# Performance work log

Hardware: AMD Instinct MI355X
Metric: run time of the kernel (lower is better)

## Reference

```python
import jax, jax.numpy as jnp
import numpy as np

INPUT_SIZE = 512
SLOT_SIZE = 256
MLP_HIDDEN = 512
NUM_SLOTS = 8
NUM_ITERS = 3
EPSILON = 1e-6
LN_EPS = 1e-5


def _layernorm(x, g, b):
    m = jnp.mean(x, axis=-1, keepdims=True)
    v = jnp.mean(jnp.square(x - m), axis=-1, keepdims=True)
    return (x - m) * jax.lax.rsqrt(v + LN_EPS) * g + b


def setup_inputs() -> dict:
    key = jax.random.key(0)
    ks = jax.random.split(key, 16)
    N, B, W = 32, 64, 24
    s = 0.02
    inp = {
        "sentence": jax.random.normal(ks[0], (N, B, W, INPUT_SIZE), jnp.float32),
        "sentence_sum": jax.random.normal(ks[1], (N, B, INPUT_SIZE), jnp.float32),
        "mask": jax.random.randint(ks[2], (N, B, W), 0, 2, jnp.int32),
        "Wk": jax.random.normal(ks[3], (INPUT_SIZE, SLOT_SIZE), jnp.float32) * s,
        "bk": jnp.zeros((SLOT_SIZE,), jnp.float32),
        "Wv": jax.random.normal(ks[4], (INPUT_SIZE, SLOT_SIZE), jnp.float32) * s,
        "bv": jnp.zeros((SLOT_SIZE,), jnp.float32),
        "Wq": jax.random.normal(ks[5], (SLOT_SIZE, SLOT_SIZE), jnp.float32) * s,
        "bq": jnp.zeros((SLOT_SIZE,), jnp.float32),
        "g_ln": jnp.ones((SLOT_SIZE,), jnp.float32),
        "b_ln": jnp.zeros((SLOT_SIZE,), jnp.float32),
        "W1": jax.random.normal(ks[6], (SLOT_SIZE, MLP_HIDDEN), jnp.float32) * s,
        "b1": jnp.zeros((MLP_HIDDEN,), jnp.float32),
        "W2": jax.random.normal(ks[7], (MLP_HIDDEN, SLOT_SIZE), jnp.float32) * s,
        "b2": jnp.zeros((SLOT_SIZE,), jnp.float32),
        "Wbind": jax.random.normal(ks[8], (INPUT_SIZE, NUM_SLOTS * SLOT_SIZE), jnp.float32) * s,
        "bbind": jnp.zeros((NUM_SLOTS * SLOT_SIZE,), jnp.float32),
        "Wproj": jax.random.normal(ks[9], (2 * SLOT_SIZE, SLOT_SIZE), jnp.float32) * s,
        "bproj": jnp.zeros((SLOT_SIZE,), jnp.float32),
    }
    return inp


def reference(sentence, sentence_sum, mask, Wk, bk, Wv, bv, Wq, bq, g_ln, b_ln,
              W1, b1, W2, b2, Wbind, bbind, Wproj, bproj):
    N, B = sentence.shape[0], sentence.shape[1]
    # initial slots from the sentence summary: [N, B, NUM_SLOTS, SLOT]
    initial_slots = (sentence_sum @ Wbind + bbind).reshape(N, B, NUM_SLOTS, SLOT_SIZE)
    # additive mask on the word axis: [N, B, W, 1]
    maskf = -1e6 * (1.0 - mask.astype(jnp.float32))[..., None]
    # elu(+1) feature maps for keys; plain linear values
    k = jax.nn.elu(sentence @ Wk + bk) + 1.0  # [N,B,W,SLOT]
    v = sentence @ Wv + bv                    # [N,B,W,SLOT]

    scale = 1.0 / SLOT_SIZE
    slots = initial_slots
    for _ in range(NUM_ITERS):
        q = (slots @ Wq + bq) + initial_slots
        q = jax.nn.elu(q * (SLOT_SIZE ** -0.5)) + 1.0  # [N,B,S,SLOT]
        attn_logits = jnp.einsum('nbis,nbjs->nbij', k, q) + maskf  # [N,B,W,S]
        attn = jax.nn.softmax(attn_logits, axis=3) + EPSILON
        attn = attn / jnp.sum(attn, axis=2, keepdims=True)  # renorm over words
        updates = jnp.einsum('nbij,nbik->nbjk', attn, v)    # [N,B,S,SLOT]
        h = _layernorm(updates, g_ln, b_ln)
        h = jax.nn.relu(h @ W1 + b1) @ W2 + b2
        slots = slots + h * scale

    # dropout is identity in eval mode
    slots = jnp.concatenate([initial_slots, slots], axis=-1)
    slots = slots @ Wproj + bproj
    return slots
```

## Files before the change

### kernel.cpp

```cpp
#include <hip/hip_runtime.h>
#include <hip/hip_bf16.h>
#include <math.h>

typedef unsigned int uint;
typedef unsigned short ushort;
typedef __attribute__((ext_vector_type(8))) short bf16x8;
typedef __attribute__((ext_vector_type(4))) float f32x4;

__device__ __forceinline__ float bu2f(ushort u){ union{uint u; float f;} v; v.u = ((uint)u)<<16; return v.f; }
__device__ __forceinline__ ushort f2bu(float x){ union{float f; uint u;} v; v.f = x; uint r = (v.u + 0x7FFFu + ((v.u>>16)&1u))>>16; return (ushort)r; }
__device__ __forceinline__ uint pack2(float a, float b){ return (uint)f2bu(a) | ((uint)f2bu(b) << 16); }
__device__ __forceinline__ uint cvtpk2(float a, float b){
    uint r; asm("v_cvt_pk_bf16_f32 %0, %1, %2" : "=v"(r) : "v"(a), "v"(b)); return r;
}

#define GEPI_IS0  0
#define GEPI_Q    2
#define GEPI_RELU 3
#define GEPI_MLP2 4
#define GEPI_OUT  5

#define SWZ(r, c) (((r) << 5) + ((((c) ^ ((r) >> 1)) & 3) << 3))

template<int EPI>
__global__ __launch_bounds__(256) void gemm64(
    const ushort* __restrict__ Abf, int lda,
    const ushort* __restrict__ Bt,
    const float* __restrict__ xb0,
    float* __restrict__ fp0,
    ushort* __restrict__ up0, ushort* __restrict__ up1,
    int M, int N, int K)
{
    __shared__ ushort As[64 * 32];
    __shared__ ushort Bs[64 * 32];
    int tid = threadIdx.x;
    int wave = tid >> 6, lane = tid & 63;
    int wr = wave >> 1, wc = wave & 1;
    int quad = lane >> 4, l15 = lane & 15;
    int row0 = blockIdx.y * 64, col0 = blockIdx.x * 64;
    int sr = tid >> 2, c4 = tid & 3, sc = c4 * 8;
    int sst = SWZ(sr, c4);

    f32x4 acc[2][2];
    #pragma unroll
    for (int i = 0; i < 2; i++)
        #pragma unroll
        for (int j = 0; j < 2; j++) acc[i][j] = (f32x4){0.f, 0.f, 0.f, 0.f};

    const ushort* Ap = Abf + (size_t)(row0 + sr) * lda + sc;
    const ushort* Bp = Bt  + (size_t)(col0 + sr) * K   + sc;
    uint4 ra = *(const uint4*)Ap;
    uint4 rb = *(const uint4*)Bp;

    for (int k0 = 0; k0 < K; k0 += 32) {
        *(uint4*)&As[sst] = ra;
        *(uint4*)&Bs[sst] = rb;
        __syncthreads();
        if (k0 + 32 < K) {
            ra = *(const uint4*)(Ap + k0 + 32);
            rb = *(const uint4*)(Bp + k0 + 32);
        }
        bf16x8 af[2], bfr[2];
        #pragma unroll
        for (int mt = 0; mt < 2; mt++) {
            int ar = wr * 32 + mt * 16 + l15;
            af[mt] = *(const bf16x8*)&As[SWZ(ar, quad)];
        }
        #pragma unroll
        for (int nt = 0; nt < 2; nt++) {
            int br = wc * 32 + nt * 16 + l15;
            bfr[nt] = *(const bf16x8*)&Bs[SWZ(br, quad)];
        }
        #pragma unroll
        for (int mt = 0; mt < 2; mt++)
            #pragma unroll
            for (int nt = 0; nt < 2; nt++)
                acc[mt][nt] = __builtin_amdgcn_mfma_f32_16x16x32_bf16(
                    af[mt], bfr[nt], acc[mt][nt], 0, 0, 0);
        __syncthreads();
    }

    #pragma unroll
    for (int mt = 0; mt < 2; mt++) {
        #pragma unroll
        for (int nt = 0; nt < 2; nt++) {
            #pragma unroll
            for (int reg = 0; reg < 4; reg++) {
                int gr = row0 + wr * 32 + mt * 16 + quad * 4 + reg;
                int gc = col0 + wc * 32 + nt * 16 + l15;
                float x = acc[mt][nt][reg] + xb0[gc];
                if (EPI == GEPI_IS0) {
                    size_t srow = (size_t)gr * 8 + (gc >> 8);
                    int dim = gc & 255;
                    fp0[srow * 256 + dim] = x;
                    ushort xb = f2bu(x);
                    up0[srow * 512 + dim]       = xb;
                    up0[srow * 512 + 256 + dim] = xb;
                } else if (EPI == GEPI_Q) {
                    float y = (x + bu2f(up1[(size_t)gr * 512 + gc])) * 0.0625f;
                    y = y > 0.f ? y + 1.f : expf(y);
                    up0[(size_t)gr * 256 + gc] = f2bu(y);
                } else if (EPI == GEPI_RELU) {
                    up0[(size_t)gr * 512 + gc] = f2bu(fmaxf(x, 0.f));
                } else if (EPI == GEPI_MLP2) {
                    size_t i = (size_t)gr * 256 + gc;
                    float s = fp0[i] + x * (1.f / 256.f);
                    fp0[i] = s;
                    up0[(size_t)gr * 512 + 256 + gc] = f2bu(s);
                } else {
                    fp0[(size_t)gr * 256 + gc] = x;
                }
            }
        }
    }
}

__global__ __launch_bounds__(256) void gemm_kv64(
    const ushort* __restrict__ A0,
    const ushort* __restrict__ A1,
    const ushort* __restrict__ Bt,
    const float* __restrict__ bk, const float* __restrict__ bv,
    ushort* __restrict__ kbuf, ushort* __restrict__ vbuf, int K)
{
    __shared__ ushort As[64 * 32];
    __shared__ ushort Bs[64 * 32];
    int tid = threadIdx.x;
    int wave = tid >> 6, lane = tid & 63;
    int wr = wave >> 1, wc = wave & 1;
    int quad = lane >> 4, l15 = lane & 15;

    int bid = blockIdx.x;
    int x8  = bid & 7;
    int tt  = bid >> 3;
    int cb  = tt & 7;
    int rb  = (tt >> 3) * 8 + x8;
    int row0 = rb * 64, col0 = cb * 64;
    int sr = tid >> 2, c4 = tid & 3, sc = c4 * 8;
    int sst = SWZ(sr, c4);

    f32x4 acc[2][2];
    #pragma unroll
    for (int i = 0; i < 2; i++)
        #pragma unroll
        for (int j = 0; j < 2; j++) acc[i][j] = (f32x4){0.f, 0.f, 0.f, 0.f};

    const ushort* Ap = (row0 < 32768)
        ? (A0 + (size_t)(row0 + sr) * K + sc)
        : (A1 + (size_t)(row0 - 32768 + sr) * K + sc);
    const ushort* Bp = Bt + (size_t)(col0 + sr) * K + sc;
    uint4 ra = *(const uint4*)Ap;
    uint4 rbv = *(const uint4*)Bp;

    for (int k0 = 0; k0 < K; k0 += 32) {
        *(uint4*)&As[sst] = ra;
        *(uint4*)&Bs[sst] = rbv;
        __syncthreads();
        if (k0 + 32 < K) {
            ra  = *(const uint4*)(Ap + k0 + 32);
            rbv = *(const uint4*)(Bp + k0 + 32);
        }
        bf16x8 af[2], bfr[2];
        #pragma unroll
        for (int mt = 0; mt < 2; mt++) {
            int ar = wr * 32 + mt * 16 + l15;
            af[mt] = *(const bf16x8*)&As[SWZ(ar, quad)];
        }
        #pragma unroll
        for (int nt = 0; nt < 2; nt++) {
            int br = wc * 32 + nt * 16 + l15;
            bfr[nt] = *(const bf16x8*)&Bs[SWZ(br, quad)];
        }
        #pragma unroll
        for (int mt = 0; mt < 2; mt++)
            #pragma unroll
            for (int nt = 0; nt < 2; nt++)
                acc[mt][nt] = __builtin_amdgcn_mfma_f32_16x16x32_bf16(
                    af[mt], bfr[nt], acc[mt][nt], 0, 0, 0);
        __syncthreads();
    }

    bool isK = (col0 < 256);
    const float* __restrict__ bias = isK ? bk : bv;
    ushort* __restrict__ outp = isK ? kbuf : vbuf;
    int cbase = isK ? col0 : col0 - 256;

    #pragma unroll
    for (int mt = 0; mt < 2; mt++) {
        #pragma unroll
        for (int nt = 0; nt < 2; nt++) {
            #pragma unroll
            for (int reg = 0; reg < 4; reg++) {
                int gr = row0 + wr * 32 + mt * 16 + quad * 4 + reg;
                int gc = cbase + wc * 32 + nt * 16 + l15;
                float x = acc[mt][nt][reg] + bias[gc];
                if (isK) x = x > 0.f ? x + 1.f : expf(x);
                outp[(size_t)gr * 256 + gc] = f2bu(x);
            }
        }
    }
}

__global__ __launch_bounds__(256) void prep_kernel(
    const float* __restrict__ sentence,
    const float* __restrict__ sent_sum,
    const float* __restrict__ Wbind, const float* __restrict__ Wk,
    const float* __restrict__ Wv, const float* __restrict__ Wq,
    const float* __restrict__ W1, const float* __restrict__ W2,
    const float* __restrict__ Wproj,
    ushort* __restrict__ sentA0, ushort* __restrict__ sentA1,
    ushort* __restrict__ ssum_bf,
    ushort* __restrict__ Wbind_t, ushort* __restrict__ Wkv_t,
    ushort* __restrict__ Wq_t, ushort* __restrict__ W1_t,
    ushort* __restrict__ W2_t, ushort* __restrict__ Wproj_t)
{
    int gid = blockIdx.x * 256 + threadIdx.x;
    if (gid < 6291456) {
        float4 f = ((const float4*)sentence)[gid];
        uint2 o; o.x = cvtpk2(f.x, f.y); o.y = cvtpk2(f.z, f.w);
        if (gid < 4194304) ((uint2*)sentA0)[gid] = o;
        else               ((uint2*)sentA1)[gid - 4194304] = o;
        return;
    }
    int idx = gid - 6291456;
    if (idx < 262144) {
        float4 f = ((const float4*)sent_sum)[idx];
        uint2 o; o.x = pack2(f.x, f.y); o.y = pack2(f.z, f.w);
        ((uint2*)ssum_bf)[idx] = o; return;
    }
    idx -= 262144;
    if (idx < 1048576) { int n = idx >> 9, k = idx & 511;
        Wbind_t[idx] = f2bu(Wbind[(size_t)k * 2048 + n]); return; }
    idx -= 1048576;
    if (idx < 262144) { int n = idx >> 9, k = idx & 511;
        Wkv_t[idx] = f2bu(n < 256 ? Wk[(size_t)k * 256 + n] : Wv[(size_t)k * 256 + n - 256]); return; }
    idx -= 262144;
    if (idx < 65536) { int n = idx >> 8, k = idx & 255;
        Wq_t[idx] = f2bu(Wq[(size_t)k * 256 + n]); return; }
    idx -= 65536;
    if (idx < 131072) { int n = idx >> 8, k = idx & 255;
        W1_t[idx] = f2bu(W1[(size_t)k * 512 + n]); return; }
    idx -= 131072;
    if (idx < 131072) { int n = idx >> 9, k = idx & 511;
        W2_t[idx] = f2bu(W2[(size_t)k * 256 + n]); return; }
    idx -= 131072;
    if (idx < 131072) { int n = idx >> 9, k = idx & 511;
        Wproj_t[idx] = f2bu(Wproj[(size_t)k * 256 + n]); return; }
}

__global__ __launch_bounds__(256) void attn_kernel(
    const ushort* __restrict__ kbuf, const ushort* __restrict__ vbuf,
    const ushort* __restrict__ qbuf, const int* __restrict__ mask,
    const float* __restrict__ g_ln, const float* __restrict__ b_ln,
    ushort* __restrict__ ubuf)
{
    const int W = 24, S = 8;
    __shared__ ushort kk[24 * 264], vv[24 * 264], qsb[8 * 264];
    __shared__ float us[8 * 257];
    __shared__ float attnw[24][8];
    __shared__ float colsum[8], mean_s[8], rstd_s[8], maskf[24];

    int nb = blockIdx.x, t = threadIdx.x;
    size_t bw = (size_t)nb * W * 256, bs = (size_t)nb * S * 256;

    for (int l = t; l < 3072; l += 256) {
        int row = l >> 7, col = l & 127;
        ((uint*)kk)[row * 132 + col] = ((const uint*)(kbuf + bw))[l];
        ((uint*)vv)[row * 132 + col] = ((const uint*)(vbuf + bw))[l];
    }
    for (int l = t; l < 1024; l += 256) {
        int row = l >> 7, col = l & 127;
        ((uint*)qsb)[row * 132 + col] = ((const uint*)(qbuf + bs))[l];
    }
    if (t < W) maskf[t] = mask[(size_t)nb * W + t] ? 0.f : -1e6f;
    __syncthreads();

    if (t < W * S) {
        int i = t >> 3, j = t & 7;
        float a = 0.f;
        for (int d0 = 0; d0 < 256; d0 += 8) {
            bf16x8 kv8 = *(const bf16x8*)&kk[i * 264 + d0];
            bf16x8 qv8 = *(const bf16x8*)&qsb[j * 264 + d0];
            #pragma unroll
            for (int m = 0; m < 8; m++)
                a += bu2f((ushort)kv8[m]) * bu2f((ushort)qv8[m]);
        }
        attnw[i][j] = a + maskf[i];
    }
    __syncthreads();

    if (t < W) {
        float m = attnw[t][0];
        #pragma unroll
        for (int j = 1; j < S; j++) m = fmaxf(m, attnw[t][j]);
        float e[S]; float s = 0.f;
        #pragma unroll
        for (int j = 0; j < S; j++) { e[j] = expf(attnw[t][j] - m); s += e[j]; }
        #pragma unroll
        for (int j = 0; j < S; j++) attnw[t][j] = e[j] / s + 1e-6f;
    }
    __syncthreads();

    if (t < S) {
        float s = 0.f;
        for (int i = 0; i < W; i++) s += attnw[i][t];
        colsum[t] = s;
    }
    __syncthreads();

    {
        float acc[S] = {};
        #pragma unroll
        for (int i = 0; i < W; i++) {
            float vx = bu2f(vv[i * 264 + t]);
            float4 w0 = *(const float4*)&attnw[i][0];
            float4 w1 = *(const float4*)&attnw[i][4];
            acc[0] += w0.x * vx; acc[1] += w0.y * vx;
            acc[2] += w0.z * vx; acc[3] += w0.w * vx;
            acc[4] += w1.x * vx; acc[5] += w1.y * vx;
            acc[6] += w1.z * vx; acc[7] += w1.w * vx;
        }
        #pragma unroll
        for (int j = 0; j < S; j++) us[j * 257 + t] = acc[j] / colsum[j];
    }
    __syncthreads();

    {
        int lane = t & 63;
        #pragma unroll
        for (int jj = 0; jj < 2; jj++) {
            int j = (t >> 6) * 2 + jj;
            float x0 = us[j * 257 + lane],       x1 = us[j * 257 + lane + 64];
            float x2 = us[j * 257 + lane + 128], x3 = us[j * 257 + lane + 192];
            float p = x0 + x1 + x2 + x3;
            for (int off = 32; off; off >>= 1) p += __shfl_xor(p, off);
            float mean = p * (1.f / 256.f);
            float d0 = x0 - mean, d1 = x1 - mean, d2 = x2 - mean, d3 = x3 - mean;
            float vr = d0 * d0 + d1 * d1 + d2 * d2 + d3 * d3;
            for (int off = 32; off; off >>= 1) vr += __shfl_xor(vr, off);
            if (lane == 0) {
                mean_s[j] = mean;
                rstd_s[j] = rsqrtf(vr * (1.f / 256.f) + 1e-5f);
            }
        }
    }
    __syncthreads();

    {
        float g = g_ln[t], bb = b_ln[t];
        #pragma unroll
        for (int j = 0; j < S; j++)
            ubuf[bs + j * 256 + t] = f2bu((us[j * 257 + t] - mean_s[j]) * rstd_s[j] * g + bb);
    }
}

__global__ __launch_bounds__(256) void mega_kernel(
    const float* __restrict__ sentence, const float* __restrict__ sent_sum,
    const int*  __restrict__ mask,
    const float* __restrict__ Wk, const float* __restrict__ bk,
    const float* __restrict__ Wv, const float* __restrict__ bv,
    const float* __restrict__ Wq, const float* __restrict__ bq,
    const float* __restrict__ g_ln, const float* __restrict__ b_ln,
    const float* __restrict__ W1, const float* __restrict__ b1,
    const float* __restrict__ W2, const float* __restrict__ b2,
    const float* __restrict__ Wbind, const float* __restrict__ bbind,
    const float* __restrict__ Wproj, const float* __restrict__ bproj,
    float* __restrict__ out)
{
    const int W = 24, S = 8, D = 256, IN = 512, H = 512;
    __shared__ float seh[2048];
    __shared__ ushort kk[24 * 256];
    __shared__ ushort vv[24 * 256];
    __shared__ float is0s[8 * 256];
    __shared__ float sl[8 * 256];
    __shared__ float qv[8 * 256];
    __shared__ float attnw[24][8];
    __shared__ float colsum[8], mean_s[8], rstd_s[8], maskf[24];

    int nb = blockIdx.x, t = threadIdx.x;
    size_t sbase = (size_t)nb * W * IN;

    if (t < W) maskf[t] = mask[(size_t)nb * W + t] ? 0.f : -1e6f;
    for (int l = t; l < IN; l += 256) seh[l] = sent_sum[(size_t)nb * IN + l];
    __syncthreads();
    {
        float acc[S];
        #pragma unroll
        for (int j = 0; j < S; j++) acc[j] = bbind[j * D + t];
        for (int c = 0; c < IN; c++) {
            float sc = seh[c];
            #pragma unroll
            for (int j = 0; j < S; j++) acc[j] += sc * Wbind[(size_t)c * (S * D) + j * D + t];
        }
        #pragma unroll
        for (int j = 0; j < S; j++) { is0s[j * D + t] = acc[j]; sl[j * D + t] = acc[j]; }
    }
    {
        float ka[W], va[W];
        float bkv = bk[t], bvv = bv[t];
        #pragma unroll
        for (int i = 0; i < W; i++) { ka[i] = bkv; va[i] = bvv; }
        for (int ch = 0; ch < 8; ch++) {
            __syncthreads();
            for (int l = t; l < W * 64; l += 256) {
                int i = l >> 6, c = l & 63;
                seh[l] = sentence[sbase + (size_t)i * IN + ch * 64 + c];
            }
            __syncthreads();
            for (int c = 0; c < 64; c++) {
                int cg = ch * 64 + c;
                float wk = Wk[(size_t)cg * D + t];
                float wv = Wv[(size_t)cg * D + t];
                #pragma unroll
                for (int i = 0; i < W; i++) {
                    float s = seh[i * 64 + c];
                    ka[i] += s * wk; va[i] += s * wv;
                }
            }
        }
        #pragma unroll
        for (int i = 0; i < W; i++) {
            float kx = ka[i];
            kk[i * D + t] = f2bu(kx > 0.f ? kx + 1.f : expf(kx));
            vv[i * D + t] = f2bu(va[i]);
        }
    }
    __syncthreads();

    for (int it = 0; it < 3; it++) {
        {
            float qa[S]; float bqv = bq[t];
            #pragma unroll
            for (int j = 0; j < S; j++) qa[j] = bqv + is0s[j * D + t];
            for (int c = 0; c < D; c++) {
                float wq = Wq[(size_t)c * D + t];
                #pragma unroll
                for (int j = 0; j < S; j++) qa[j] += sl[j * D + c] * wq;
            }
            #pragma unroll
            for (int j = 0; j < S; j++) {
                float y = qa[j] * 0.0625f;
                qv[j * D + t] = y > 0.f ? y + 1.f : expf(y);
            }
        }
        __syncthreads();
        if (t < W * S) {
            int i = t >> 3, j = t & 7;
            float a = 0.f;
            #pragma unroll 8
            for (int d = 0; d < D; d++) a += bu2f(kk[i * D + d]) * qv[j * D + d];
            attnw[i][j] = a + maskf[i];
        }
        __syncthreads();
        if (t < W) {
            float m = attnw[t][0];
            #pragma unroll
            for (int j = 1; j < S; j++) m = fmaxf(m, attnw[t][j]);
            float e[S]; float s = 0.f;
            #pragma unroll
            for (int j = 0; j < S; j++) { e[j] = expf(attnw[t][j] - m); s += e[j]; }
            #pragma unroll
            for (int j = 0; j < S; j++) attnw[t][j] = e[j] / s + 1e-6f;
        }
        __syncthreads();
        if (t < S) {
            float s = 0.f;
            for (int i = 0; i < W; i++) s += attnw[i][t];
            colsum[t] = s;
        }
        __syncthreads();
        {
            float acc[S] = {};
            #pragma unroll
            for (int i = 0; i < W; i++) {
                float vx = bu2f(vv[i * D + t]);
                #pragma unroll
                for (int j = 0; j < S; j++) acc[j] += attnw[i][j] * vx;
            }
            #pragma unroll
            for (int j = 0; j < S; j++) qv[j * D + t] = acc[j] / colsum[j];
        }
        __syncthreads();
        {
            int lane = t & 63;
            #pragma unroll
            for (int jj = 0; jj < 2; jj++) {
                int j = (t >> 6) * 2 + jj;
                float x0 = qv[j * D + lane],       x1 = qv[j * D + lane + 64];
                float x2 = qv[j * D + lane + 128], x3 = qv[j * D + lane + 192];
                float p = x0 + x1 + x2 + x3;
                for (int off = 32; off; off >>= 1) p += __shfl_xor(p, off);
                float mean = p * (1.f / 256.f);
                float d0 = x0 - mean, d1 = x1 - mean, d2 = x2 - mean, d3 = x3 - mean;
                float vr = d0 * d0 + d1 * d1 + d2 * d2 + d3 * d3;
                for (int off = 32; off; off >>= 1) vr += __shfl_xor(vr, off);
                if (lane == 0) { mean_s[j] = mean; rstd_s[j] = rsqrtf(vr * (1.f / 256.f) + 1e-5f); }
            }
        }
        __syncthreads();
        {
            float g = g_ln[t], bb = b_ln[t];
            #pragma unroll
            for (int j = 0; j < S; j++)
                qv[j * D + t] = (qv[j * D + t] - mean_s[j]) * rstd_s[j] * g + bb;
        }
        __syncthreads();
        {
            float sa[S]; float b2v = b2[t];
            #pragma unroll
            for (int j = 0; j < S; j++) sa[j] = b2v;
            for (int half = 0; half < 2; half++) {
                int hcol = half * 256 + t;
                float ha[S]; float b1v = b1[hcol];
                #pragma unroll
                for (int j = 0; j < S; j++) ha[j] = b1v;
                for (int d = 0; d < D; d++) {
                    float w1 = W1[(size_t)d * H + hcol];
                    #pragma unroll
                    for (int j = 0; j < S; j++) ha[j] += qv[j * D + d] * w1;
                }
                __syncthreads();
                #pragma unroll
                for (int j = 0; j < S; j++) seh[j * D + t] = fmaxf(ha[j], 0.f);
                __syncthreads();
                for (int h = 0; h < 256; h++) {
                    float w2 = W2[(size_t)(half * 256 + h) * D + t];
                    #pragma unroll
                    for (int j = 0; j < S; j++) sa[j] += seh[j * D + h] * w2;
                }
            }
            __syncthreads();
            #pragma unroll
            for (int j = 0; j < S; j++) sl[j * D + t] += sa[j] * (1.f / 256.f);
        }
        __syncthreads();
    }
    {
        float oa[S]; float bpv = bproj[t];
        #pragma unroll
        for (int j = 0; j < S; j++) oa[j] = bpv;
        for (int c = 0; c < D; c++) {
            float wp1 = Wproj[(size_t)c * D + t];
            float wp2 = Wproj[(size_t)(D + c) * D + t];
            #pragma unroll
            for (int j = 0; j < S; j++)
                oa[j] += is0s[j * D + c] * wp1 + sl[j * D + c] * wp2;
        }
        #pragma unroll
        for (int j = 0; j < S; j++)
            out[(size_t)nb * (S * D) + j * D + t] = oa[j];
    }
}

extern "C" void kernel_launch(void* const* d_in, const int* in_sizes, int n_in,
                              void* d_out, int out_size, void* d_ws, size_t ws_size,
                              hipStream_t stream)
{
    const float* sentence = (const float*)d_in[0];
    const float* sent_sum = (const float*)d_in[1];
    const int*  mask      = (const int*)d_in[2];
    const float* Wk = (const float*)d_in[3];  const float* bk = (const float*)d_in[4];
    const float* Wv = (const float*)d_in[5];  const float* bv = (const float*)d_in[6];
    const float* Wq = (const float*)d_in[7];  const float* bq = (const float*)d_in[8];
    const float* g_ln = (const float*)d_in[9];  const float* b_ln = (const float*)d_in[10];
    const float* W1 = (const float*)d_in[11]; const float* b1 = (const float*)d_in[12];
    const float* W2 = (const float*)d_in[13]; const float* b2 = (const float*)d_in[14];
    const float* Wbind = (const float*)d_in[15]; const float* bbind = (const float*)d_in[16];
    const float* Wproj = (const float*)d_in[17]; const float* bproj = (const float*)d_in[18];
    float* out = (float*)d_out;

    const size_t WS_NEEDED = 123076608ULL;
    if (ws_size >= WS_NEEDED) {
        char* w = (char*)d_ws;
        float*  slots   = (float*) (w);
        ushort* catb    = (ushort*)(w + 16777216);
        ushort* kbuf    = (ushort*)(w + 33554432);
        ushort* vbuf    = (ushort*)(w + 58720256);
        ushort* qbuf    = (ushort*)(w + 83886080);
        ushort* ubuf    = (ushort*)(w + 92274688);
        ushort* hbuf    = (ushort*)(w + 100663296);
        ushort* ssum_bf = (ushort*)(w + 117440512);
        ushort* Wbind_t = (ushort*)(w + 119537664);
        ushort* Wkv_t   = (ushort*)(w + 121634816);
        ushort* Wq_t    = (ushort*)(w + 122159104);
        ushort* W1_t    = (ushort*)(w + 122290176);
        ushort* W2_t    = (ushort*)(w + 122552320);
        ushort* Wproj_t = (ushort*)(w + 122814464);

        ushort* sentA0 = (ushort*)(w);
        ushort* sentA1 = (ushort*)(w + 83886080);

        prep_kernel<<<dim3(32512), dim3(256), 0, stream>>>(
            sentence, sent_sum, Wbind, Wk, Wv, Wq, W1, W2, Wproj,
            sentA0, sentA1,
            ssum_bf, Wbind_t, Wkv_t, Wq_t, W1_t, W2_t, Wproj_t);

        gemm_kv64<<<dim3(6144), dim3(256), 0, stream>>>(
            sentA0, sentA1, Wkv_t, bk, bv, kbuf, vbuf, 512);

        gemm64<GEPI_IS0><<<dim3(32, 32), dim3(256), 0, stream>>>(
            ssum_bf, 512, Wbind_t, bbind,
            slots, catb, nullptr, 2048, 2048, 512);

        for (int it = 0; it < 3; it++) {
            gemm64<GEPI_Q><<<dim3(4, 256), dim3(256), 0, stream>>>(
                catb + 256, 512, Wq_t, bq,
                nullptr, qbuf, catb, 16384, 256, 256);
            attn_kernel<<<dim3(2048), dim3(256), 0, stream>>>(
                kbuf, vbuf, qbuf, mask, g_ln, b_ln, ubuf);
            gemm64<GEPI_RELU><<<dim3(8, 256), dim3(256), 0, stream>>>(
                ubuf, 256, W1_t, b1,
                nullptr, hbuf, nullptr, 16384, 512, 256);
            gemm64<GEPI_MLP2><<<dim3(4, 256), dim3(256), 0, stream>>>(
                hbuf, 512, W2_t, b2,
                slots, catb, nullptr, 16384, 256, 512);
        }

        gemm64<GEPI_OUT><<<dim3(4, 256), dim3(256), 0, stream>>>(
            catb, 512, Wproj_t, bproj,
            out, nullptr, nullptr, 16384, 256, 512);
    } else {
        mega_kernel<<<dim3(2048), dim3(256), 0, stream>>>(
            sentence, sent_sum, mask, Wk, bk, Wv, bv, Wq, bq, g_ln, b_ln,
            W1, b1, W2, b2, Wbind, bbind, Wproj, bproj, out);
    }
}
```

Before: 497.9 us.

## Fuse the two MLP GEMMs into one kernel keeping hidden activations in LDS

Replaces the separate W1+ReLU GEMM and W2+residual GEMM with a single kernel per 32-row tile. The 512-wide hidden activation is held in shared memory instead of being written to and re-read from global memory, and one launch is saved per iteration. The final iteration also skips writing the fp32 slots back. In exchange, weights are read straight from global memory without LDS staging, and the grid shrinks to 512 blocks with 48KB of LDS each, which may lower occupancy and raise weight-load traffic.

Measured after the change: 544.5 us. 9.4% more time.

```diff
diff --git a/kernel.cpp b/kernel.cpp
--- a/kernel.cpp
+++ b/kernel.cpp
@@ -115,6 +115,108 @@
     }
 }
 
+template<bool LAST>
+__global__ __launch_bounds__(256) void mlp_fused(
+    const ushort* __restrict__ ubuf,
+    const ushort* __restrict__ W1t,
+    const float*  __restrict__ b1,
+    const ushort* __restrict__ W2t,
+    const float*  __restrict__ b2,
+    float* __restrict__ slots,
+    ushort* __restrict__ catb)
+{
+    __shared__ ushort uL[8][1024];
+    __shared__ ushort hL[16][1024];
+    int tid = threadIdx.x;
+    int wave = tid >> 6, lane = tid & 63;
+    int quad = lane >> 4, l15 = lane & 15;
+    int row0 = blockIdx.x * 32;
+
+    for (int l = tid; l < 1024; l += 256) {
+        int r = l >> 5, cc = l & 31;
+        uint4 v = *(const uint4*)(ubuf + (size_t)(row0 + r) * 256 + cc * 8);
+        *(uint4*)&uL[cc >> 2][SWZ(r, cc & 3)] = v;
+    }
+    __syncthreads();
+
+    {
+        int n0 = wave * 128;
+        f32x4 acc[2][8];
+        #pragma unroll
+        for (int i = 0; i < 2; i++)
+            #pragma unroll
+            for (int j = 0; j < 8; j++) acc[i][j] = (f32x4){0.f, 0.f, 0.f, 0.f};
+
+        #pragma unroll
+        for (int kc = 0; kc < 8; kc++) {
+            bf16x8 a0 = *(const bf16x8*)&uL[kc][SWZ(l15, quad)];
+            bf16x8 a1 = *(const bf16x8*)&uL[kc][SWZ(16 + l15, quad)];
+            #pragma unroll
+            for (int nt = 0; nt < 8; nt++) {
+                bf16x8 b = *(const bf16x8*)(W1t +
+                    (size_t)(n0 + nt * 16 + l15) * 256 + kc * 32 + quad * 8);
+                acc[0][nt] = __builtin_amdgcn_mfma_f32_16x16x32_bf16(a0, b, acc[0][nt], 0, 0, 0);
+                acc[1][nt] = __builtin_amdgcn_mfma_f32_16x16x32_bf16(a1, b, acc[1][nt], 0, 0, 0);
+            }
+        }
+        #pragma unroll
+        for (int nt = 0; nt < 8; nt++) {
+            int col = n0 + nt * 16 + l15;
+            float b1v = b1[col];
+            int kc2 = col >> 5, base = SWZ(0, (col >> 3) & 3) + (col & 7);
+            #pragma unroll
+            for (int mt = 0; mt < 2; mt++) {
+                #pragma unroll
+                for (int reg = 0; reg < 4; reg++) {
+                    int row = mt * 16 + quad * 4 + reg;
+                    float x = fmaxf(acc[mt][nt][reg] + b1v, 0.f);
+                    hL[kc2][SWZ(row, (col >> 3) & 3) + (col & 7)] = f2bu(x);
+                }
+            }
+            (void)base;
+        }
+    }
+    __syncthreads();
+
+    {
+        int n0 = wave * 64;
+        f32x4 acc[2][4];
+        #pragma unroll
+        for (int i = 0; i < 2; i++)
+            #pragma unroll
+            for (int j = 0; j < 4; j++) acc[i][j] = (f32x4){0.f, 0.f, 0.f, 0.f};
+
+        #pragma unroll
+        for (int kc = 0; kc < 16; kc++) {
+            bf16x8 a0 = *(const bf16x8*)&hL[kc][SWZ(l15, quad)];
+            bf16x8 a1 = *(const bf16x8*)&hL[kc][SWZ(16 + l15, quad)];
+            #pragma unroll
+            for (int nt = 0; nt < 4; nt++) {
+                bf16x8 b = *(const bf16x8*)(W2t +
+                    (size_t)(n0 + nt * 16 + l15) * 512 + kc * 32 + quad * 8);
+                acc[0][nt] = __builtin_amdgcn_mfma_f32_16x16x32_bf16(a0, b, acc[0][nt], 0, 0, 0);
+                acc[1][nt] = __builtin_amdgcn_mfma_f32_16x16x32_bf16(a1, b, acc[1][nt], 0, 0, 0);
+            }
+        }
+        #pragma unroll
+        for (int nt = 0; nt < 4; nt++) {
+            int gc = n0 + nt * 16 + l15;
+            float b2v = b2[gc];
+            #pragma unroll
+            for (int mt = 0; mt < 2; mt++) {
+                #pragma unroll
+                for (int reg = 0; reg < 4; reg++) {
+                    int gr = row0 + mt * 16 + quad * 4 + reg;
+                    size_t i = (size_t)gr * 256 + gc;
+                    float s = slots[i] + (acc[mt][nt][reg] + b2v) * (1.f / 256.f);
+                    if (!LAST) slots[i] = s;
+                    catb[(size_t)gr * 512 + 256 + gc] = f2bu(s);
+                }
+            }
+        }
+    }
+}
+
 __global__ __launch_bounds__(256) void gemm_kv64(
     const ushort* __restrict__ A0,
     const ushort* __restrict__ A1,
@@ -577,7 +679,6 @@
         ushort* vbuf    = (ushort*)(w + 58720256);
         ushort* qbuf    = (ushort*)(w + 83886080);
         ushort* ubuf    = (ushort*)(w + 92274688);
-        ushort* hbuf    = (ushort*)(w + 100663296);
         ushort* ssum_bf = (ushort*)(w + 117440512);
         ushort* Wbind_t = (ushort*)(w + 119537664);
         ushort* Wkv_t   = (ushort*)(w + 121634816);
@@ -607,12 +708,12 @@
                 nullptr, qbuf, catb, 16384, 256, 256);
             attn_kernel<<<dim3(2048), dim3(256), 0, stream>>>(
                 kbuf, vbuf, qbuf, mask, g_ln, b_ln, ubuf);
-            gemm64<GEPI_RELU><<<dim3(8, 256), dim3(256), 0, stream>>>(
-                ubuf, 256, W1_t, b1,
-                nullptr, hbuf, nullptr, 16384, 512, 256);
-            gemm64<GEPI_MLP2><<<dim3(4, 256), dim3(256), 0, stream>>>(
-                hbuf, 512, W2_t, b2,
-                slots, catb, nullptr, 16384, 256, 512);
+            if (it < 2)
+                mlp_fused<false><<<dim3(512), dim3(256), 0, stream>>>(
+                    ubuf, W1_t, b1, W2_t, b2, slots, catb);
+            else
+                mlp_fused<true><<<dim3(512), dim3(256), 0, stream>>>(
+                    ubuf, W1_t, b1, W2_t, b2, slots, catb);
         }
 
         gemm64<GEPI_OUT><<<dim3(4, 256), dim3(256), 0, stream>>>(
```
